# Kernel tuning notes

Measured on AMD Instinct MI355X. Metric: run time of the kernel, lower is better.

The kernel has to match this reference:

```python
import jax, jax.numpy as jnp
import numpy as np

B, T, D_IN = 32, 128, 32
H1, H, PEN = 1024, 2048, 1024  # linear1 out, GRU hidden, penultimate
C, P = 64, 4                   # cultivars, phenos


def setup_inputs() -> dict:
    key = jax.random.key(0)
    ks = jax.random.split(key, 22)
    s = 0.02
    inp = {}
    inp['x'] = jax.random.normal(ks[0], (B, T, D_IN), dtype=jnp.float32)
    inp['cultivar_label'] = jax.random.randint(ks[1], (B, 1), 0, C)
    inp['W1'] = jax.random.normal(ks[2], (H1, D_IN), dtype=jnp.float32) * s
    inp['b1'] = jnp.zeros((H1,), jnp.float32)
    inp['W2'] = jax.random.normal(ks[3], (H, H1), dtype=jnp.float32) * s
    inp['b2'] = jnp.zeros((H,), jnp.float32)
    # GRU weights, PyTorch layout: gates stacked (r,z,n) along dim 0
    inp['W_ih'] = jax.random.normal(ks[4], (3 * H, H), dtype=jnp.float32) * s
    inp['b_ih'] = jnp.zeros((3 * H,), jnp.float32)
    inp['W_hh'] = jax.random.normal(ks[5], (3 * H, H), dtype=jnp.float32) * s
    inp['b_hh'] = jnp.zeros((3 * H,), jnp.float32)
    inp['W3'] = jax.random.normal(ks[6], (PEN, H), dtype=jnp.float32) * s
    inp['b3'] = jnp.zeros((PEN,), jnp.float32)
    # per-cultivar expert heads (each a Linear(PEN, 1)) packed as tables
    inp['W4'] = jax.random.normal(ks[7], (C, PEN), dtype=jnp.float32) * s
    inp['b4'] = jnp.zeros((C,), jnp.float32)
    inp['W5'] = jax.random.normal(ks[8], (C, PEN), dtype=jnp.float32) * s
    inp['b5'] = jnp.zeros((C,), jnp.float32)
    inp['W6'] = jax.random.normal(ks[9], (C, PEN), dtype=jnp.float32) * s
    inp['b6'] = jnp.zeros((C,), jnp.float32)
    inp['Wp'] = jax.random.normal(ks[10], (P, C, PEN), dtype=jnp.float32) * s
    inp['bp'] = jnp.zeros((P, C), jnp.float32)
    return inp


def _gru(x_seq, W_ih, b_ih, W_hh, b_hh):
    # x_seq: [B,T,H]; PyTorch GRU gate order (r, z, n)
    Bd, Hd = x_seq.shape[0], W_hh.shape[1]
    xp = jnp.einsum('bth,gh->btg', x_seq, W_ih) + b_ih  # [B,T,3H]

    def step(h, xp_t):
        hp = h @ W_hh.T + b_hh
        xr, xz, xn = jnp.split(xp_t, 3, axis=-1)
        hr, hz, hn = jnp.split(hp, 3, axis=-1)
        r = jax.nn.sigmoid(xr + hr)
        z = jax.nn.sigmoid(xz + hz)
        n = jnp.tanh(xn + r * hn)
        h_new = (1.0 - z) * n + z * h
        return h_new, h_new

    h0 = jnp.zeros((Bd, Hd), x_seq.dtype)
    _, hs = jax.lax.scan(step, h0, jnp.swapaxes(xp, 0, 1))  # [T,B,H]
    return jnp.swapaxes(hs, 0, 1)  # [B,T,H]


def reference(x, cultivar_label, W1, b1, W2, b2, W_ih, b_ih, W_hh, b_hh,
              W3, b3, W4, b4, W5, b5, W6, b6, Wp, bp):
    out = jax.nn.relu(jnp.einsum('btd,hd->bth', x, W1) + b1)
    out = jax.nn.relu(jnp.einsum('bth,gh->btg', out, W2) + b2)
    out = _gru(out, W_ih, b_ih, W_hh, b_hh)
    out_s = jax.nn.relu(jnp.einsum('bth,ph->btp', out, W3) + b3)  # [B,T,PEN]
    labels = cultivar_label[:, 0]

    def head(W, b):  # gather expert row per sample -> [B,T,1]
        return (jnp.einsum('btd,bd->bt', out_s, W[labels]) + b[labels][:, None])[..., None]

    out_lt_10 = head(W4, b4)
    out_lt_50 = head(W5, b5)
    out_lt_90 = head(W6, b6)
    # pheno heads: Wp[:, labels] -> [P,B,PEN]
    out_ph = jax.nn.sigmoid(
        jnp.einsum('btd,pbd->pbt', out_s, Wp[:, labels]) + bp[:, labels][:, :, None]
    )[..., None]  # [P,B,T,1]
    return (out_lt_10, out_lt_50, out_lt_90, out_ph, 0)
```

## Files before the change

kernel.cpp:

```cpp
#include <hip/hip_runtime.h>
#include <hip/hip_bf16.h>
#include <math.h>


typedef __bf16 bf16_t;
typedef __bf16 bf16x8 __attribute__((ext_vector_type(8)));
typedef float  f32x4  __attribute__((ext_vector_type(4)));

static __device__ __forceinline__ void zero4(f32x4& v) {
  v[0] = 0.0f; v[1] = 0.0f; v[2] = 0.0f; v[3] = 0.0f;
}

template <typename T>
static __device__ __forceinline__ bf16x8 load8_as_bf16(const T* p);
template <>
__device__ __forceinline__ bf16x8 load8_as_bf16<bf16_t>(const bf16_t* p) {
  return *(const bf16x8*)p;
}
template <>
__device__ __forceinline__ bf16x8 load8_as_bf16<float>(const float* p) {
  bf16x8 v;
#pragma unroll
  for (int u = 0; u < 8; ++u) v[u] = (bf16_t)p[u];
  return v;
}

template <typename TA, typename TB>
__global__ __launch_bounds__(256) void gemm_bt(
    const TA* __restrict__ A, const TB* __restrict__ Bm,
    const float* __restrict__ bias, bf16_t* __restrict__ C,
    int M, int N, int K, int relu)
{
  __shared__ __align__(16) bf16_t As[128 * 32];
  __shared__ __align__(16) bf16_t Bs[128 * 32];

  const int tid  = threadIdx.x;
  const int lane = tid & 63;
  const int wave = tid >> 6;
  const int q    = lane >> 4;
  const int l15  = lane & 15;
  const int wr   = wave >> 1;
  const int wc   = wave & 1;
  const int m0   = blockIdx.y * 128;
  const int n0   = blockIdx.x * 128;

  f32x4 acc[4][4];
#pragma unroll
  for (int i = 0; i < 4; ++i)
#pragma unroll
    for (int j = 0; j < 4; ++j) zero4(acc[i][j]);

  const int se = wave * 512 + lane * 8;

  const int kt_count = K >> 5;
  for (int kt = 0; kt < kt_count; ++kt) {
    const int k0 = kt << 5;

    bf16x8 av[2], bv[2];
#pragma unroll
    for (int c = 0; c < 2; ++c) {
      const int e   = c * 2048 + se;
      const int row = e >> 5;
      const int col = e & 31;
      av[c] = load8_as_bf16<TA>(&A [(size_t)(m0 + row) * K + k0 + col]);
      bv[c] = load8_as_bf16<TB>(&Bm[(size_t)(n0 + row) * K + k0 + col]);
    }

    __syncthreads();
#pragma unroll
    for (int c = 0; c < 2; ++c) {
      *(bf16x8*)&As[c * 2048 + se] = av[c];
      *(bf16x8*)&Bs[c * 2048 + se] = bv[c];
    }
    __syncthreads();

    bf16x8 af[4], bfv[4];
#pragma unroll
    for (int i = 0; i < 4; ++i)
      af[i] = *(const bf16x8*)&As[(wr * 64 + i * 16 + l15) * 32 + q * 8];
#pragma unroll
    for (int j = 0; j < 4; ++j)
      bfv[j] = *(const bf16x8*)&Bs[(wc * 64 + j * 16 + l15) * 32 + q * 8];

#pragma unroll
    for (int i = 0; i < 4; ++i)
#pragma unroll
      for (int j = 0; j < 4; ++j)
        acc[i][j] = __builtin_amdgcn_mfma_f32_16x16x32_bf16(af[i], bfv[j], acc[i][j], 0, 0, 0);
  }

#pragma unroll
  for (int j = 0; j < 4; ++j) {
    const int n = n0 + wc * 64 + j * 16 + l15;
    const float bvl = bias[n];
#pragma unroll
    for (int i = 0; i < 4; ++i) {
      const int mbase = m0 + wr * 64 + i * 16 + q * 4;
#pragma unroll
      for (int r = 0; r < 4; ++r) {
        float v = acc[i][j][r] + bvl;
        if (relu) v = v > 0.0f ? v : 0.0f;
        C[(size_t)(mbase + r) * N + n] = (bf16_t)v;
      }
    }
  }
}

__global__ __launch_bounds__(512, 2) void gru_persistent(
    const float* __restrict__ W_hh, const float* __restrict__ b_hh,
    const bf16_t* __restrict__ xp, bf16_t* __restrict__ hs,
    unsigned* __restrict__ arr)
{
  __shared__ __align__(16) float hp_p[8][32][52];

  const int tid  = threadIdx.x;
  const int lane = tid & 63;
  const int wave = tid >> 6;
  const int q    = lane >> 4;
  const int l15  = lane & 15;
  const int j0   = blockIdx.x * 16;
  const int k0w  = wave * 256;

  bf16x8 wf[3][8];
#pragma unroll
  for (int rt = 0; rt < 3; ++rt) {
    const float* rp = W_hh + ((size_t)(rt * 2048 + j0 + l15)) * 2048 + k0w;
#pragma unroll
    for (int win = 0; win < 8; ++win)
      wf[rt][win] = load8_as_bf16<float>(rp + win * 32 + q * 8);
  }

  const int b  = tid >> 4;
  const int jj = tid & 15;
  const int jg = j0 + jj;
  const float bh_r = b_hh[jg];
  const float bh_z = b_hh[2048 + jg];
  const float bh_n = b_hh[4096 + jg];

  float hcur = 0.0f;
  unsigned* hs32 = (unsigned*)hs;

  float xr_c = (float)xp[(size_t)(b * 128 + 0) * 6144 + jg];
  float xz_c = (float)xp[(size_t)(b * 128 + 0) * 6144 + 2048 + jg];
  float xn_c = (float)xp[(size_t)(b * 128 + 0) * 6144 + 4096 + jg];

  for (int t = 0; t < 128; ++t) {
    if (t > 0) {
      bf16x8 bfr[2][8];
#pragma unroll
      for (int ct = 0; ct < 2; ++ct) {
        const bf16_t* bp_ = hs + ((size_t)(ct * 16 + l15) * 128 + (t - 1)) * 2048
                               + k0w + q * 8;
#pragma unroll
        for (int win = 0; win < 8; ++win)
          bfr[ct][win] = *(const bf16x8*)(bp_ + win * 32);
      }

      f32x4 acc[3][2];
#pragma unroll
      for (int rt = 0; rt < 3; ++rt)
#pragma unroll
        for (int ct = 0; ct < 2; ++ct) zero4(acc[rt][ct]);

#pragma unroll
      for (int win = 0; win < 8; ++win)
#pragma unroll
        for (int rt = 0; rt < 3; ++rt)
#pragma unroll
          for (int ct = 0; ct < 2; ++ct)
            acc[rt][ct] = __builtin_amdgcn_mfma_f32_16x16x32_bf16(
                wf[rt][win], bfr[ct][win], acc[rt][ct], 0, 0, 0);

#pragma unroll
      for (int rt = 0; rt < 3; ++rt)
#pragma unroll
        for (int ct = 0; ct < 2; ++ct)
          *(f32x4*)&hp_p[wave][ct * 16 + l15][rt * 16 + q * 4] = acc[rt][ct];
    }
    __syncthreads();

    float pr = 0.0f, pz = 0.0f, pn = 0.0f;
    if (t > 0) {
#pragma unroll
      for (int w = 0; w < 8; ++w) {
        pr += hp_p[w][b][jj];
        pz += hp_p[w][b][16 + jj];
        pn += hp_p[w][b][32 + jj];
      }
    }
    const float r_ = 1.0f / (1.0f + __expf(-(xr_c + pr + bh_r)));
    const float z_ = 1.0f / (1.0f + __expf(-(xz_c + pz + bh_z)));
    const float aa = xn_c + r_ * (pn + bh_n);
    const float et = __expf(-2.0f * aa);
    const float n_ = (1.0f - et) / (1.0f + et);
    hcur = (1.0f - z_) * n_ + z_ * hcur;

    union { bf16_t h; unsigned short u; } cv; cv.h = (bf16_t)hcur;
    const unsigned hv = cv.u;
    const unsigned ov = (unsigned)__shfl_xor((int)hv, 1, 64);
    if ((tid & 1) == 0) {
      const unsigned pk = hv | (ov << 16);
      const size_t widx = ((size_t)b * 128 + t) * 1024 + (jg >> 1);
      __hip_atomic_store(hs32 + widx, pk, __ATOMIC_RELAXED,
                         __HIP_MEMORY_SCOPE_AGENT);
    }

    if (t < 127) {
      asm volatile("s_waitcnt vmcnt(0)" ::: "memory");
      __syncthreads();
      if (tid == 0)
        __hip_atomic_store(arr + (size_t)t * 128 + blockIdx.x, 1u,
                           __ATOMIC_RELAXED, __HIP_MEMORY_SCOPE_AGENT);
      const int tn = t + 1;
      const float xr_n = (float)xp[(size_t)(b * 128 + tn) * 6144 + jg];
      const float xz_n = (float)xp[(size_t)(b * 128 + tn) * 6144 + 2048 + jg];
      const float xn_n = (float)xp[(size_t)(b * 128 + tn) * 6144 + 4096 + jg];

      const unsigned long long* f64p =
          (const unsigned long long*)(arr + (size_t)t * 128) + wave * 8;
      const unsigned long long tgt = 0x0000000100000001ull;
      int guard = 0;
      for (;;) {
        unsigned long long v = tgt;
        if (lane < 8)
          v = __hip_atomic_load(f64p + lane, __ATOMIC_RELAXED,
                                __HIP_MEMORY_SCOPE_AGENT);
        if (__all(v == tgt)) break;
        __builtin_amdgcn_s_sleep(1);
        if (++guard > (1 << 20)) break;
      }

      xr_c = xr_n; xz_c = xz_n; xn_c = xn_n;
    }
  }
}

__global__ __launch_bounds__(256) void heads_kernel(
    const bf16_t* __restrict__ out_s, const int* __restrict__ labels,
    const float* __restrict__ W4, const float* __restrict__ b4,
    const float* __restrict__ W5, const float* __restrict__ b5,
    const float* __restrict__ W6, const float* __restrict__ b6,
    const float* __restrict__ Wp, const float* __restrict__ bp,
    float* __restrict__ out)
{
  const int bt  = blockIdx.x;
  const int b   = bt >> 7;
  const int lab = labels[b];
  const bf16_t* os  = out_s + (size_t)bt * 1024;
  const float* w4  = W4 + (size_t)lab * 1024;
  const float* w5  = W5 + (size_t)lab * 1024;
  const float* w6  = W6 + (size_t)lab * 1024;
  const float* wp0 = Wp + (size_t)lab * 1024;

  float s[7] = {0, 0, 0, 0, 0, 0, 0};
  for (int d = threadIdx.x; d < 1024; d += 256) {
    const float v = (float)os[d];
    s[0] += v * w4[d];
    s[1] += v * w5[d];
    s[2] += v * w6[d];
    s[3] += v * wp0[d];
    s[4] += v * wp0[65536 + d];
    s[5] += v * wp0[131072 + d];
    s[6] += v * wp0[196608 + d];
  }
#pragma unroll
  for (int i = 0; i < 7; ++i)
    for (int off = 32; off > 0; off >>= 1)
      s[i] += __shfl_down(s[i], off, 64);

  __shared__ float red[4][7];
  const int lane = threadIdx.x & 63, wave = threadIdx.x >> 6;
  if (lane == 0)
    for (int i = 0; i < 7; ++i) red[wave][i] = s[i];
  __syncthreads();
  if (threadIdx.x == 0) {
    float tsum[7];
    for (int i = 0; i < 7; ++i)
      tsum[i] = red[0][i] + red[1][i] + red[2][i] + red[3][i];
    out[bt]        = tsum[0] + b4[lab];
    out[4096 + bt] = tsum[1] + b5[lab];
    out[8192 + bt] = tsum[2] + b6[lab];
#pragma unroll
    for (int p = 0; p < 4; ++p) {
      const float v = tsum[3 + p] + bp[p * 64 + lab];
      out[12288 + p * 4096 + bt] = 1.0f / (1.0f + __expf(-v));
    }
  }
}

extern "C" void kernel_launch(void* const* d_in, const int* in_sizes, int n_in,
                              void* d_out, int out_size, void* d_ws, size_t ws_size,
                              hipStream_t stream)
{
  const float* x     = (const float*)d_in[0];
  const int*   label = (const int*)d_in[1];
  const float* W1    = (const float*)d_in[2];
  const float* b1    = (const float*)d_in[3];
  const float* W2    = (const float*)d_in[4];
  const float* b2    = (const float*)d_in[5];
  const float* W_ih  = (const float*)d_in[6];
  const float* b_ih  = (const float*)d_in[7];
  const float* W_hh  = (const float*)d_in[8];
  const float* b_hh  = (const float*)d_in[9];
  const float* W3    = (const float*)d_in[10];
  const float* b3    = (const float*)d_in[11];
  const float* W4    = (const float*)d_in[12];
  const float* b4    = (const float*)d_in[13];
  const float* W5    = (const float*)d_in[14];
  const float* b5    = (const float*)d_in[15];
  const float* W6    = (const float*)d_in[16];
  const float* b6    = (const float*)d_in[17];
  const float* Wp    = (const float*)d_in[18];
  const float* bp    = (const float*)d_in[19];

  char* ws = (char*)d_ws;
  unsigned* arr = (unsigned*)ws;
  bf16_t* out1  = (bf16_t*)(ws + (24u << 20));
  bf16_t* out2  = (bf16_t*)(ws + (32u << 20));
  bf16_t* xp    = (bf16_t*)(ws + (48u << 20));
  bf16_t* hs    = (bf16_t*)(ws + (24u << 20));
  bf16_t* out_s = (bf16_t*)(ws + (40u << 20));
  float*  outp  = (float*)d_out;

  hipMemsetAsync(d_out, 0, (size_t)out_size * sizeof(float), stream);
  hipMemsetAsync(ws, 0, 65536, stream);

  dim3 blk(256);
  gemm_bt<float, float><<<dim3(8, 32), blk, 0, stream>>>(x, W1, b1, out1, 4096, 1024, 32, 1);
  gemm_bt<bf16_t, float><<<dim3(16, 32), blk, 0, stream>>>(out1, W2, b2, out2, 4096, 2048, 1024, 1);
  gemm_bt<bf16_t, float><<<dim3(48, 32), blk, 0, stream>>>(out2, W_ih, b_ih, xp, 4096, 6144, 2048, 0);
  {
    void* gru_args[] = { (void*)&W_hh, (void*)&b_hh, (void*)&xp, (void*)&hs,
                         (void*)&arr };
    hipLaunchCooperativeKernel((void*)gru_persistent, dim3(128), dim3(512),
                               gru_args, 0, stream);
  }
  gemm_bt<bf16_t, float><<<dim3(8, 32), blk, 0, stream>>>(hs, W3, b3, out_s, 4096, 1024, 2048, 1);
  heads_kernel<<<dim3(4096), blk, 0, stream>>>(out_s, label, W4, b4, W5, b5, W6, b6, Wp, bp, outp);
}
```

Measured before the change: 1.440 ms.

## Split persistent GRU over 256 blocks with W_hh slices held in LDS

```diff
diff --git a/kernel.cpp b/kernel.cpp
--- a/kernel.cpp
+++ b/kernel.cpp
@@ -4,6 +4,7 @@
 
 
 typedef __bf16 bf16_t;
+typedef __bf16 bf16x4 __attribute__((ext_vector_type(4)));
 typedef __bf16 bf16x8 __attribute__((ext_vector_type(8)));
 typedef float  f32x4  __attribute__((ext_vector_type(4)));
 
@@ -106,43 +107,59 @@
   }
 }
 
+#define WROW 2056
+
 __global__ __launch_bounds__(512, 2) void gru_persistent(
     const float* __restrict__ W_hh, const float* __restrict__ b_hh,
     const bf16_t* __restrict__ xp, bf16_t* __restrict__ hs,
     unsigned* __restrict__ arr)
 {
-  __shared__ __align__(16) float hp_p[8][32][52];
+  __shared__ __align__(16) bf16_t Ws[24 * WROW];
+  __shared__ __align__(16) float hp_p[8][32][28];
 
   const int tid  = threadIdx.x;
   const int lane = tid & 63;
   const int wave = tid >> 6;
   const int q    = lane >> 4;
   const int l15  = lane & 15;
-  const int j0   = blockIdx.x * 16;
+  const int j0   = blockIdx.x * 8;
   const int k0w  = wave * 256;
 
-  bf16x8 wf[3][8];
-#pragma unroll
-  for (int rt = 0; rt < 3; ++rt) {
-    const float* rp = W_hh + ((size_t)(rt * 2048 + j0 + l15)) * 2048 + k0w;
-#pragma unroll
-    for (int win = 0; win < 8; ++win)
-      wf[rt][win] = load8_as_bf16<float>(rp + win * 32 + q * 8);
-  }
-
-  const int b  = tid >> 4;
-  const int jj = tid & 15;
+  for (int m = 0; m < 24; ++m) {
+    const int gate = m >> 3;
+    const float* src = W_hh + (size_t)(gate * 2048 + j0 + (m & 7)) * 2048;
+    const int c = tid * 4;
+    bf16x4 v;
+#pragma unroll
+    for (int u = 0; u < 4; ++u) v[u] = (bf16_t)src[c + u];
+    *(bf16x4*)&Ws[m * WROW + c] = v;
+  }
+
+  const bool pw = tid < 256;
+  const int b  = (tid >> 3) & 31;
+  const int jj = tid & 7;
   const int jg = j0 + jj;
-  const float bh_r = b_hh[jg];
-  const float bh_z = b_hh[2048 + jg];
-  const float bh_n = b_hh[4096 + jg];
+  float bh_r = 0.f, bh_z = 0.f, bh_n = 0.f;
+  if (pw) {
+    bh_r = b_hh[jg];
+    bh_z = b_hh[2048 + jg];
+    bh_n = b_hh[4096 + jg];
+  }
+
+  const bf16_t* arow0 = &Ws[(size_t)l15 * WROW + k0w];
+  const bf16_t* arow1 = &Ws[(size_t)(16 + (l15 & 7)) * WROW + k0w];
 
   float hcur = 0.0f;
   unsigned* hs32 = (unsigned*)hs;
 
-  float xr_c = (float)xp[(size_t)(b * 128 + 0) * 6144 + jg];
-  float xz_c = (float)xp[(size_t)(b * 128 + 0) * 6144 + 2048 + jg];
-  float xn_c = (float)xp[(size_t)(b * 128 + 0) * 6144 + 4096 + jg];
+  float xr_c = 0.f, xz_c = 0.f, xn_c = 0.f;
+  if (pw) {
+    xr_c = (float)xp[(size_t)(b * 128 + 0) * 6144 + jg];
+    xz_c = (float)xp[(size_t)(b * 128 + 0) * 6144 + 2048 + jg];
+    xn_c = (float)xp[(size_t)(b * 128 + 0) * 6144 + 4096 + jg];
+  }
+
+  __syncthreads();
 
   for (int t = 0; t < 128; ++t) {
     if (t > 0) {
@@ -156,73 +173,81 @@
           bfr[ct][win] = *(const bf16x8*)(bp_ + win * 32);
       }
 
-      f32x4 acc[3][2];
-#pragma unroll
-      for (int rt = 0; rt < 3; ++rt)
+      f32x4 acc[2][2];
+#pragma unroll
+      for (int rt = 0; rt < 2; ++rt)
 #pragma unroll
         for (int ct = 0; ct < 2; ++ct) zero4(acc[rt][ct]);
 
 #pragma unroll
-      for (int win = 0; win < 8; ++win)
-#pragma unroll
-        for (int rt = 0; rt < 3; ++rt)
-#pragma unroll
-          for (int ct = 0; ct < 2; ++ct)
-            acc[rt][ct] = __builtin_amdgcn_mfma_f32_16x16x32_bf16(
-                wf[rt][win], bfr[ct][win], acc[rt][ct], 0, 0, 0);
-
-#pragma unroll
-      for (int rt = 0; rt < 3; ++rt)
-#pragma unroll
-        for (int ct = 0; ct < 2; ++ct)
-          *(f32x4*)&hp_p[wave][ct * 16 + l15][rt * 16 + q * 4] = acc[rt][ct];
+      for (int win = 0; win < 8; ++win) {
+        const bf16x8 a0 = *(const bf16x8*)(arow0 + win * 32 + q * 8);
+        const bf16x8 a1 = *(const bf16x8*)(arow1 + win * 32 + q * 8);
+        acc[0][0] = __builtin_amdgcn_mfma_f32_16x16x32_bf16(a0, bfr[0][win], acc[0][0], 0, 0, 0);
+        acc[0][1] = __builtin_amdgcn_mfma_f32_16x16x32_bf16(a0, bfr[1][win], acc[0][1], 0, 0, 0);
+        acc[1][0] = __builtin_amdgcn_mfma_f32_16x16x32_bf16(a1, bfr[0][win], acc[1][0], 0, 0, 0);
+        acc[1][1] = __builtin_amdgcn_mfma_f32_16x16x32_bf16(a1, bfr[1][win], acc[1][1], 0, 0, 0);
+      }
+
+#pragma unroll
+      for (int ct = 0; ct < 2; ++ct) {
+        *(f32x4*)&hp_p[wave][ct * 16 + l15][q * 4] = acc[0][ct];
+        if (q < 2)
+          *(f32x4*)&hp_p[wave][ct * 16 + l15][16 + q * 4] = acc[1][ct];
+      }
     }
     __syncthreads();
 
-    float pr = 0.0f, pz = 0.0f, pn = 0.0f;
-    if (t > 0) {
-#pragma unroll
-      for (int w = 0; w < 8; ++w) {
-        pr += hp_p[w][b][jj];
-        pz += hp_p[w][b][16 + jj];
-        pn += hp_p[w][b][32 + jj];
-      }
-    }
-    const float r_ = 1.0f / (1.0f + __expf(-(xr_c + pr + bh_r)));
-    const float z_ = 1.0f / (1.0f + __expf(-(xz_c + pz + bh_z)));
-    const float aa = xn_c + r_ * (pn + bh_n);
-    const float et = __expf(-2.0f * aa);
-    const float n_ = (1.0f - et) / (1.0f + et);
-    hcur = (1.0f - z_) * n_ + z_ * hcur;
-
-    union { bf16_t h; unsigned short u; } cv; cv.h = (bf16_t)hcur;
-    const unsigned hv = cv.u;
-    const unsigned ov = (unsigned)__shfl_xor((int)hv, 1, 64);
-    if ((tid & 1) == 0) {
-      const unsigned pk = hv | (ov << 16);
-      const size_t widx = ((size_t)b * 128 + t) * 1024 + (jg >> 1);
-      __hip_atomic_store(hs32 + widx, pk, __ATOMIC_RELAXED,
-                         __HIP_MEMORY_SCOPE_AGENT);
+    if (pw) {
+      float pr = 0.0f, pz = 0.0f, pn = 0.0f;
+      if (t > 0) {
+#pragma unroll
+        for (int w = 0; w < 8; ++w) {
+          pr += hp_p[w][b][jj];
+          pz += hp_p[w][b][8 + jj];
+          pn += hp_p[w][b][16 + jj];
+        }
+      }
+      const float r_ = 1.0f / (1.0f + __expf(-(xr_c + pr + bh_r)));
+      const float z_ = 1.0f / (1.0f + __expf(-(xz_c + pz + bh_z)));
+      const float aa = xn_c + r_ * (pn + bh_n);
+      const float et = __expf(-2.0f * aa);
+      const float n_ = (1.0f - et) / (1.0f + et);
+      hcur = (1.0f - z_) * n_ + z_ * hcur;
+
+      union { bf16_t h; unsigned short u; } cv; cv.h = (bf16_t)hcur;
+      const unsigned hv = cv.u;
+      const unsigned ov = (unsigned)__shfl_xor((int)hv, 1, 64);
+      if ((tid & 1) == 0) {
+        const unsigned pk = hv | (ov << 16);
+        const size_t widx = ((size_t)b * 128 + t) * 1024 + (jg >> 1);
+        __hip_atomic_store(hs32 + widx, pk, __ATOMIC_RELAXED,
+                           __HIP_MEMORY_SCOPE_AGENT);
+      }
     }
 
     if (t < 127) {
       asm volatile("s_waitcnt vmcnt(0)" ::: "memory");
       __syncthreads();
       if (tid == 0)
-        __hip_atomic_store(arr + (size_t)t * 128 + blockIdx.x, 1u,
+        __hip_atomic_store(arr + (size_t)t * 256 + blockIdx.x, 1u,
                            __ATOMIC_RELAXED, __HIP_MEMORY_SCOPE_AGENT);
       const int tn = t + 1;
-      const float xr_n = (float)xp[(size_t)(b * 128 + tn) * 6144 + jg];
-      const float xz_n = (float)xp[(size_t)(b * 128 + tn) * 6144 + 2048 + jg];
-      const float xn_n = (float)xp[(size_t)(b * 128 + tn) * 6144 + 4096 + jg];
+      float xr_n = 0.f, xz_n = 0.f, xn_n = 0.f;
+      if (pw) {
+        xr_n = (float)xp[(size_t)(b * 128 + tn) * 6144 + jg];
+        xz_n = (float)xp[(size_t)(b * 128 + tn) * 6144 + 2048 + jg];
+        xn_n = (float)xp[(size_t)(b * 128 + tn) * 6144 + 4096 + jg];
+      }
+      asm volatile("" ::: "memory");
 
       const unsigned long long* f64p =
-          (const unsigned long long*)(arr + (size_t)t * 128) + wave * 8;
+          (const unsigned long long*)(arr + (size_t)t * 256) + wave * 16;
       const unsigned long long tgt = 0x0000000100000001ull;
       int guard = 0;
       for (;;) {
         unsigned long long v = tgt;
-        if (lane < 8)
+        if (lane < 16)
           v = __hip_atomic_load(f64p + lane, __ATOMIC_RELAXED,
                                 __HIP_MEMORY_SCOPE_AGENT);
         if (__all(v == tgt)) break;
@@ -323,7 +348,7 @@
   float*  outp  = (float*)d_out;
 
   hipMemsetAsync(d_out, 0, (size_t)out_size * sizeof(float), stream);
-  hipMemsetAsync(ws, 0, 65536, stream);
+  hipMemsetAsync(ws, 0, 131072, stream);
 
   dim3 blk(256);
   gemm_bt<float, float><<<dim3(8, 32), blk, 0, stream>>>(x, W1, b1, out1, 4096, 1024, 32, 1);
@@ -332,7 +357,7 @@
   {
     void* gru_args[] = { (void*)&W_hh, (void*)&b_hh, (void*)&xp, (void*)&hs,
                          (void*)&arr };
-    hipLaunchCooperativeKernel((void*)gru_persistent, dim3(128), dim3(512),
+    hipLaunchCooperativeKernel((void*)gru_persistent, dim3(256), dim3(512),
                                gru_args, 0, stream);
   }
   gemm_bt<bf16_t, float><<<dim3(8, 32), blk, 0, stream>>>(hs, W3, b3, out_s, 4096, 1024, 2048, 1);
```

Result: slower. 1.484 ms (+3.1%).
